# Performance work log

Measured on AMD Instinct MI355X. Metric: run time of the kernel, lower is better.

Reference implementation:

```python
import jax, jax.numpy as jnp
import numpy as np

HEADS, HEAD_SIZE, FREQS, MAX_PERIOD = 16, 64, 256, 10000
D_MODEL = 1024
NEG_INF = -1e9


def sinusoid_embedding(seq_len, frequencies, max_period):
    # Interleaved sin/cos sinusoid table, shape (seq_len, frequencies).
    pos = np.arange(seq_len, dtype=np.float64)[:, None]
    idx = np.arange(frequencies)[None, :]
    inv_freq = max_period ** (-(idx // 2 * 2) / frequencies)
    angle = pos * inv_freq
    table = np.where(idx % 2 == 0, np.sin(angle), np.cos(angle))
    return table.astype(np.float32)


def relative_causal(scores):
    # scores: (b, n, q, v) with v indexing relative distance d = q - k.
    # Returns a[..., q, k] = scores[..., q, q - k] (k > q entries are masked later).
    L = scores.shape[-1]
    d = jnp.clip(jnp.arange(L)[:, None] - jnp.arange(L)[None, :], 0, L - 1)  # (q, k)
    return jnp.take_along_axis(scores, d[None, None, :, :], axis=-1)


def setup_inputs() -> dict:
    key = jax.random.key(0)
    ks = jax.random.split(key, 4)
    u = np.sqrt(3.0)
    inp = jax.random.normal(ks[0], (2, 2048, D_MODEL), dtype=jnp.float32)
    qkv = jax.random.uniform(ks[1], (D_MODEL, 3, HEADS, HEAD_SIZE), jnp.float32, -u, u)
    q_bias = jnp.zeros((HEADS, HEAD_SIZE), jnp.float32)
    positional = jax.random.uniform(ks[2], (FREQS, HEADS, HEAD_SIZE), jnp.float32, -u, u)
    out_kernel = jax.random.uniform(ks[3], (HEADS * HEAD_SIZE, D_MODEL), jnp.float32, -u, u)
    out_bias = jnp.zeros((D_MODEL,), jnp.float32)
    return {"input": inp, "qkv": qkv, "q_bias": q_bias, "positional": positional,
            "out_kernel": out_kernel, "out_bias": out_bias}


def reference(input, qkv, q_bias, positional, out_kernel, out_bias):
    b, s, x = input.shape
    n, h = HEADS, HEAD_SIZE
    # QKV projection with unit-scaling forward factor.
    w = qkv * (3.0 * x * h * n) ** -0.25
    q, k, v = jnp.einsum('bsx,xAnh->Abnsh', input, w)  # each (b, n, s, h)
    q = q + q_bias[:, None, :]
    # Content scores.
    a = jnp.einsum('bnqh,bnkh->bnqk', q, k) * h ** -0.5
    # Relative-positional scores (Transformer-XL style).
    sins = jnp.asarray(np.sqrt(2.0) * sinusoid_embedding(s, FREQS, MAX_PERIOD))
    emb = jnp.einsum('sf,fnh->nsh', sins, positional * FREQS ** -0.5)
    pos_scores = jnp.einsum('bnqh,nvh->bnqv', q, emb) * h ** -0.5
    a = a + relative_causal(pos_scores)
    # Causal mask + softmax.
    mask = jnp.tril(jnp.ones((s, s), dtype=bool))
    a = jax.nn.softmax(jnp.where(mask, a, NEG_INF), axis=-1)
    # Weighted sum and output projection (Dense, scale_for='both').
    o = jnp.einsum('bnqk,bnkh->bqnh', a, v).reshape(b, s, n * h)
    fan_in, fan_out = out_kernel.shape
    out = o @ (out_kernel * (fan_in * fan_out) ** -0.25) + out_bias
    return out
```

## Files before the change

### kernel.cpp

```cpp
#include <hip/hip_runtime.h>
#include <math.h>

#define BATCH 2
#define SEQ 2048
#define DMODEL 1024
#define HEADS 16
#define HSIZE 64
#define FREQS 256
#define NH 1024
#define QKVN 3072

typedef __bf16 bf16;
typedef __bf16 bf16x8 __attribute__((ext_vector_type(8)));
typedef float f32x4 __attribute__((ext_vector_type(4)));

static __device__ __forceinline__ unsigned short bf16_bits(float v) {
    bf16 b = (bf16)v; return __builtin_bit_cast(unsigned short, b);
}

static __device__ __forceinline__ void gload16(const void* g, void* l) {
    __builtin_amdgcn_global_load_lds(
        (const __attribute__((address_space(1))) unsigned int*)g,
        (__attribute__((address_space(3))) unsigned int*)l, 16, 0, 0);
}

__global__ __launch_bounds__(256) void prep_kernel(
    const float* __restrict__ inp, const float* __restrict__ qkv_w,
    const float* __restrict__ out_kernel, const float* __restrict__ positional,
    bf16* __restrict__ a_bf, bf16* __restrict__ wt_qkv,
    bf16* __restrict__ wt_out, bf16* __restrict__ wt_pos,
    bf16* __restrict__ sins_bf)
{
    __shared__ float tile[32][33];
    const int id = blockIdx.x, t = threadIdx.x;

    if (id < 4096) {
        int i = id * 256 + t;
        float4 v = ((const float4*)inp)[i];
        ushort4 o;
        o.x = bf16_bits(v.x); o.y = bf16_bits(v.y);
        o.z = bf16_bits(v.z); o.w = bf16_bits(v.w);
        ((ushort4*)a_bf)[i] = o;
        return;
    }
    if (id < 6144) {
        int i = (id - 4096) * 256 + t;
        int s = i >> 8, f = i & 255;
        double e = -(double)((f >> 1) << 1) / (double)FREQS;
        double invf = pow(10000.0, e);
        double ang = (double)s * invf;
        double v = (f & 1) ? cos(ang) : sin(ang);
        sins_bf[i] = (bf16)(float)(1.4142135623730951 * v);
        return;
    }
    int id2 = id - 6144;
    const float* src; bf16* dst; int R, C, c0, r0;
    if (id2 < 3072) {
        src = qkv_w; dst = wt_qkv; R = 1024; C = 3072;
        c0 = (id2 % 96) * 32; r0 = (id2 / 96) * 32;
    } else if (id2 < 4096) {
        id2 -= 3072;
        src = out_kernel; dst = wt_out; R = 1024; C = 1024;
        c0 = (id2 & 31) * 32; r0 = (id2 >> 5) * 32;
    } else {
        id2 -= 4096;
        src = positional; dst = wt_pos; R = 256; C = 1024;
        c0 = (id2 & 31) * 32; r0 = (id2 >> 5) * 32;
    }
    const int tx = t & 31, ty = t >> 5;
#pragma unroll
    for (int i = 0; i < 4; i++)
        tile[ty + i * 8][tx] = src[(size_t)(r0 + ty + i * 8) * C + c0 + tx];
    __syncthreads();
#pragma unroll
    for (int i = 0; i < 4; i++)
        dst[(size_t)(c0 + ty + i * 8) * R + r0 + tx] = (bf16)tile[tx][ty + i * 8];
}

template<int EPI>
__global__ __launch_bounds__(256) void mfma_gemm(
    const bf16* __restrict__ A, const bf16* __restrict__ Bt,
    int K, float alpha, const float* __restrict__ bias,
    float* __restrict__ outf, bf16* __restrict__ ob0, bf16* __restrict__ ob1,
    bf16* __restrict__ ob2,
    const bf16* __restrict__ A2, const bf16* __restrict__ Bt2,
    bf16* __restrict__ ob3, float alpha2)
{
    __shared__ __align__(16) bf16 Atile[2][128 * 32];
    __shared__ __align__(16) bf16 Btile[2][128 * 32];

    const int t    = threadIdx.x;
    const int lane = t & 63;
    const int w    = t >> 6;
    const int quad = lane >> 4;
    const int l16  = lane & 15;
    const int wm   = (w >> 1) * 64;
    const int wn   = (w & 1) * 64;

    bool embp = false;
    int m0 = blockIdx.y * 128, n0 = blockIdx.x * 128, Kl = K;
    const bf16* Ap = A; const bf16* Btp = Bt; float al = alpha;
    if constexpr (EPI == 1) {
        if (blockIdx.x >= 24) {
            if (blockIdx.y >= 16) return;
            embp = true;
            n0 = (blockIdx.x - 24) * 128;
            Kl = FREQS; Ap = A2; Btp = Bt2; al = alpha2;
        }
    }
    const bool swapv = (EPI == 1) && !embp && (n0 >= 2048);

    const int rS = t >> 2;
    const int cS = (t & 3) ^ ((rS >> 1) & 3);
    const bf16* ag0 = Ap  + (size_t)(m0 + rS) * Kl + cS * 8;
    const bf16* ag1 = ag0 + (size_t)64 * Kl;
    const bf16* bg0 = Btp + (size_t)(n0 + rS) * Kl + cS * 8;
    const bf16* bg1 = bg0 + (size_t)64 * Kl;

    int aoff[4], boff[4];
#pragma unroll
    for (int mi = 0; mi < 4; ++mi) {
        int r = wm + mi * 16 + l16;
        aoff[mi] = r * 32 + ((quad ^ ((r >> 1) & 3)) * 8);
    }
#pragma unroll
    for (int ni = 0; ni < 4; ++ni) {
        int r = wn + ni * 16 + l16;
        boff[ni] = r * 32 + ((quad ^ ((r >> 1) & 3)) * 8);
    }

    gload16(ag0, (char*)Atile[0] + t * 16);
    gload16(ag1, (char*)Atile[0] + 4096 + t * 16);
    gload16(bg0, (char*)Btile[0] + t * 16);
    gload16(bg1, (char*)Btile[0] + 4096 + t * 16);

    const int nK = Kl >> 5;
    f32x4 acc[4][4] = {};

    for (int kk = 0; kk < nK; ++kk) {
        __syncthreads();
        if (kk + 1 < nK) {
            ag0 += 32; ag1 += 32; bg0 += 32; bg1 += 32;
            char* ad = (char*)Atile[(kk + 1) & 1];
            char* bd = (char*)Btile[(kk + 1) & 1];
            gload16(ag0, ad + t * 16); gload16(ag1, ad + 4096 + t * 16);
            gload16(bg0, bd + t * 16); gload16(bg1, bd + 4096 + t * 16);
        }
        const bf16* ab = Atile[kk & 1];
        const bf16* bb = Btile[kk & 1];
        bf16x8 af[4], bfr[4];
#pragma unroll
        for (int mi = 0; mi < 4; ++mi) af[mi] = *(const bf16x8*)(ab + aoff[mi]);
#pragma unroll
        for (int ni = 0; ni < 4; ++ni) bfr[ni] = *(const bf16x8*)(bb + boff[ni]);

        if (!swapv) {
#pragma unroll
            for (int mi = 0; mi < 4; ++mi)
#pragma unroll
                for (int ni = 0; ni < 4; ++ni)
                    acc[mi][ni] = __builtin_amdgcn_mfma_f32_16x16x32_bf16(
                        af[mi], bfr[ni], acc[mi][ni], 0, 0, 0);
        } else {
#pragma unroll
            for (int mi = 0; mi < 4; ++mi)
#pragma unroll
                for (int ni = 0; ni < 4; ++ni)
                    acc[mi][ni] = __builtin_amdgcn_mfma_f32_16x16x32_bf16(
                        bfr[ni], af[mi], acc[mi][ni], 0, 0, 0);
        }
    }

    if constexpr (EPI == 0) {
#pragma unroll
        for (int mi = 0; mi < 4; ++mi)
#pragma unroll
            for (int ni = 0; ni < 4; ++ni) {
                int col = n0 + wn + ni * 16 + l16;
                float bb = bias[col];
#pragma unroll
                for (int rg = 0; rg < 4; ++rg) {
                    int row = m0 + wm + mi * 16 + quad * 4 + rg;
                    outf[(size_t)row * NH + col] = acc[mi][ni][rg] * al + bb;
                }
            }
    } else {
        if (embp) {
#pragma unroll
            for (int mi = 0; mi < 4; ++mi)
#pragma unroll
                for (int ni = 0; ni < 4; ++ni) {
                    int col = n0 + wn + ni * 16 + l16;
                    int head = col >> 6, h = col & 63;
#pragma unroll
                    for (int rg = 0; rg < 4; ++rg) {
                        int d = m0 + wm + mi * 16 + quad * 4 + rg;
                        int hs = h ^ (((d + 63) & 7) << 3);
                        ob3[((size_t)(head * SEQ + d)) * 64 + hs] =
                            (bf16)(acc[mi][ni][rg] * al);
                    }
                }
        } else if (n0 >= 2048) {
#pragma unroll
            for (int mi = 0; mi < 4; ++mi)
#pragma unroll
                for (int ni = 0; ni < 4; ++ni) {
                    int mcol = m0 + wm + mi * 16 + l16;
                    int bb = mcol >> 11, s = mcol & 2047;
#pragma unroll
                    for (int rg = 0; rg < 4; ++rg) {
                        int hg = n0 + wn + ni * 16 + quad * 4 + rg;
                        int head = (hg & 1023) >> 6, h = hg & 63;
                        int ss = s ^ ((h & 7) << 3);
                        ob2[((size_t)((bb * 16 + head) * 64 + h)) * SEQ + ss] =
                            (bf16)(acc[mi][ni][rg] * al);
                    }
                }
        } else {
            const int whichk = (n0 >= 1024);
#pragma unroll
            for (int mi = 0; mi < 4; ++mi)
#pragma unroll
                for (int ni = 0; ni < 4; ++ni) {
                    int cg   = (n0 + wn + ni * 16 + l16) & 1023;
                    int head = cg >> 6, h = cg & 63;
                    float qbv = whichk ? 0.0f : bias[cg];
#pragma unroll
                    for (int rg = 0; rg < 4; ++rg) {
                        int row = m0 + wm + mi * 16 + quad * 4 + rg;
                        int bb = row >> 11, s = row & 2047;
                        float v = acc[mi][ni][rg] * al;
                        if (whichk) {
                            int hs = h ^ ((s & 7) << 3);
                            ob1[((size_t)((bb * 16 + head) * SEQ + s)) * 64 + hs] = (bf16)v;
                        } else {
                            ob0[((size_t)((bb * 16 + head) * SEQ + s)) * 64 + h] =
                                (bf16)((v + qbv) * 0.125f);
                        }
                    }
                }
        }
    }
}

__device__ const unsigned char YQC[24]  = {15,15,7,14,14,13,13,6,12,12,11,11,
                                           5,10,10,9,9,4,8,8,3,2,1,0};
__device__ const unsigned char YPRT[24] = {0,1,2,0,1,0,1,2,0,1,0,1,
                                           2,0,1,0,1,2,0,1,2,2,2,2};

__global__ __launch_bounds__(256, 2) void attn_kernel(
    const bf16* __restrict__ Qb, const bf16* __restrict__ Kb,
    const bf16* __restrict__ Vtb, const bf16* __restrict__ Eb,
    bf16* __restrict__ o, float* __restrict__ Opart, float* __restrict__ Lpart)
{
    __shared__ __align__(16) bf16 Ks[2][4096];
    __shared__ __align__(16) bf16 Vts[2][4096];
    __shared__ __align__(16) bf16 Es[256 * 64];
    __shared__ __align__(16) bf16 PS[4][16][72];

    const int t    = threadIdx.x;
    const int lane = t & 63;
    const int w    = t >> 6;
    const int quad = lane >> 4;
    const int l16  = lane & 15;

    const int bx = blockIdx.x;
    const int b  = bx >> 4, n = bx & 15;
    const int yy = blockIdx.y;
    const int qc = YQC[yy];
    const int pr = YPRT[yy];
    const int q0 = qc * 128;
    const int KT = 2 * qc + 2;
    const int kt0 = (pr == 1) ? (qc + 1) : 0;
    const int kt1 = (pr == 0) ? (qc + 1) : KT;
    const bool haspeel = (pr != 0);
    const bool split   = (pr != 2);
    const int qw0 = q0 + 16 * w;
    const int qw1 = qw0 + 64;

    const bf16* __restrict__ Qp = Qb  + (size_t)bx * SEQ * 64;
    const bf16* __restrict__ Kp = Kb  + (size_t)bx * SEQ * 64;
    const bf16* __restrict__ Vp = Vtb + (size_t)bx * SEQ * 64;
    const bf16* __restrict__ Ep = Eb  + (size_t)n  * SEQ * 64;

    const int key8 = (l16 & 7) << 3;
    const int ec0  = ((quad * 8) ^ key8) * 2;
    const int ec1  = ((32 + quad * 8) ^ key8) * 2;

    bf16x8 qf[2][2];
    qf[0][0] = *(const bf16x8*)(Qp + (size_t)(qw0 + l16) * 64 + quad * 8);
    qf[0][1] = *(const bf16x8*)(Qp + (size_t)(qw0 + l16) * 64 + 32 + quad * 8);
    qf[1][0] = *(const bf16x8*)(Qp + (size_t)(qw1 + l16) * 64 + quad * 8);
    qf[1][1] = *(const bf16x8*)(Qp + (size_t)(qw1 + l16) * 64 + 32 + quad * 8);

    int dsta[4];
    bool condp[4];
#pragma unroll
    for (int rg = 0; rg < 4; ++rg) {
        int rr   = quad * 4 + rg;
        int l16c = (rr + 15 - l16) & 15;
        dsta[rg]  = ((lane & 48) + l16c) << 2;
        condp[rg] = rr > l16c;
    }

    f32x4 O[2][4] = {};
    float lsum[2][4] = {};

    {
        const bf16* ksrc = Kp + kt0 * 4096;
        char* kd = (char*)Ks[kt0 & 1];
        char* vd = (char*)Vts[kt0 & 1];
        gload16(ksrc + t * 8,        kd + t * 16);
        gload16(ksrc + 2048 + t * 8, kd + 4096 + t * 16);
        gload16(Vp + (size_t)(t >> 3) * SEQ + kt0 * 64 + (t & 7) * 8,        vd + t * 16);
        gload16(Vp + (size_t)((t >> 3) + 32) * SEQ + kt0 * 64 + (t & 7) * 8, vd + 4096 + t * 16);
        const long D0 = (long)q0 - 64 * kt0 - 63;
        const int rI0 = (-64 * kt0) & 255;
#pragma unroll
        for (int g = 0; g < 6; ++g) {
            const int sI = (rI0 + 32 * g) & 255;
            gload16(Ep + (D0 + 32 * g) * 64 + t * 8, (char*)Es + sI * 128 + t * 16);
        }
    }

    auto load_kv = [&](const char* kb, const char* vb,
                       bf16x8 (&kf)[4][2], bf16x8 (&vf)[4][2]) {
#pragma unroll
        for (int j = 0; j < 4; ++j) {
            const char* kp = kb + (j * 16 + l16) * 128;
            kf[j][0] = *(const bf16x8*)(kp + ec0);
            kf[j][1] = *(const bf16x8*)(kp + ec1);
            const char* vp = vb + (j * 16 + l16) * 128;
            vf[j][0] = *(const bf16x8*)(vp + ec0);
            vf[j][1] = *(const bf16x8*)(vp + ec1);
        }
    };
    auto eread = [&](int rb, bf16x8 (&ef)[5][2]) {
#pragma unroll
        for (int jj = 0; jj < 5; ++jj) {
            const char* ep = (const char*)Es + ((rb + 16 * jj + l16) & 255) * 128;
            ef[jj][0] = *(const bf16x8*)(ep + ec0);
            ef[jj][1] = *(const bf16x8*)(ep + ec1);
        }
    };
    auto qkmfma = [&](const bf16x8 (&q2)[2], const bf16x8 (&kf)[4][2],
                      f32x4 (&S)[4]) {
#pragma unroll
        for (int j = 0; j < 4; ++j) {
            f32x4 a = {0, 0, 0, 0};
            a = __builtin_amdgcn_mfma_f32_16x16x32_bf16(q2[1], kf[j][1], a, 0, 0, 0);
            a = __builtin_amdgcn_mfma_f32_16x16x32_bf16(q2[0], kf[j][0], a, 0, 0, 0);
            S[j] = a;
        }
    };
    auto pamfma = [&](const bf16x8 (&q2)[2], const bf16x8 (&ef)[5][2],
                      f32x4 (&pa)[5]) {
#pragma unroll
        for (int jj = 0; jj < 5; ++jj) {
            f32x4 a = {0, 0, 0, 0};
            a = __builtin_amdgcn_mfma_f32_16x16x32_bf16(q2[1], ef[jj][1], a, 0, 0, 0);
            a = __builtin_amdgcn_mfma_f32_16x16x32_bf16(q2[0], ef[jj][0], a, 0, 0, 0);
            pa[jj] = a;
        }
    };
    auto smax = [&](int kq, f32x4 (&S)[4], const f32x4 (&pa)[5], float (&ls)[4]) {
#pragma unroll
        for (int j = 0; j < 4; ++j) {
#pragma unroll
            for (int rg = 0; rg < 4; ++rg) {
                float vsel = condp[rg] ? pa[4 - j][rg] : pa[3 - j][rg];
                int pv = __builtin_amdgcn_ds_permute(dsta[rg], __float_as_int(vsel));
                float sv = S[j][rg] + __int_as_float(pv);
                bool valid = (j * 16 + l16) <= (kq + quad * 4 + rg);
                S[j][rg] = valid ? __expf(sv) : 0.0f;
            }
        }
#pragma unroll
        for (int rg = 0; rg < 4; ++rg)
            ls[rg] += S[0][rg] + S[1][rg] + S[2][rg] + S[3][rg];
    };
    auto ps_write = [&](const f32x4 (&S)[4]) {
#pragma unroll
        for (int j = 0; j < 4; ++j)
#pragma unroll
            for (int rg = 0; rg < 4; ++rg)
                PS[w][quad * 4 + rg][j * 16 + l16] = (bf16)S[j][rg];
    };
    auto pvmfma = [&](const bf16x8 (&vf)[4][2], f32x4 (&Oc)[4]) {
        bf16x8 pf0 = *(const bf16x8*)(&PS[w][l16][quad * 8]);
        bf16x8 pf1 = *(const bf16x8*)(&PS[w][l16][32 + quad * 8]);
#pragma unroll
        for (int j4 = 0; j4 < 4; ++j4) {
            Oc[j4] = __builtin_amdgcn_mfma_f32_16x16x32_bf16(pf1, vf[j4][1], Oc[j4], 0, 0, 0);
            Oc[j4] = __builtin_amdgcn_mfma_f32_16x16x32_bf16(pf0, vf[j4][0], Oc[j4], 0, 0, 0);
        }
    };

    const int ktE = kt1 - (haspeel ? 1 : 0);
    for (int kt = kt0; kt < ktE; ++kt) {
        const int k0 = kt * 64;
        __syncthreads();

        const int nt = kt + 1;
        if (nt < kt1) {
            bf16* kd = Ks[nt & 1];
            bf16* vd = Vts[nt & 1];
            const bf16* ksrc = Kp + nt * 4096;
            gload16(ksrc + t * 8,        (char*)kd + t * 16);
            gload16(ksrc + 2048 + t * 8, (char*)kd + 4096 + t * 16);
            gload16(Vp + (size_t)(t >> 3) * SEQ + nt * 64 + (t & 7) * 8,
                    (char*)vd + t * 16);
            gload16(Vp + (size_t)((t >> 3) + 32) * SEQ + nt * 64 + (t & 7) * 8,
                    (char*)vd + 4096 + t * 16);
            const long d0 = (long)q0 - nt * 64 - 63;
            const int rI = (-64 * nt) & 255;
            gload16(Ep + d0 * 64 + t * 8,        (char*)Es + rI * 128 + t * 16);
            gload16(Ep + (d0 + 32) * 64 + t * 8, (char*)Es + rI * 128 + 4096 + t * 16);
        }

        bf16x8 kf[4][2], vf[4][2];
        load_kv((const char*)Ks[kt & 1], (const char*)Vts[kt & 1], kf, vf);

        bf16x8 ef0[5][2];
        eread(16 * w - k0, ef0);
        f32x4 S0[4], pa0[5];
        __builtin_amdgcn_s_setprio(1);
        qkmfma(qf[0], kf, S0);
        pamfma(qf[0], ef0, pa0);
        __builtin_amdgcn_s_setprio(0);
        smax(qw0 - k0, S0, pa0, lsum[0]);

        bf16x8 ef1[5][2];
        eread(16 * w + 64 - k0, ef1);
        ps_write(S0);

        f32x4 S1[4], pa1[5];
        __builtin_amdgcn_s_setprio(1);
        qkmfma(qf[1], kf, S1);
        pamfma(qf[1], ef1, pa1);
        pvmfma(vf, O[0]);
        __builtin_amdgcn_s_setprio(0);

        smax(qw1 - k0, S1, pa1, lsum[1]);
        ps_write(S1);
        __builtin_amdgcn_s_setprio(1);
        pvmfma(vf, O[1]);
        __builtin_amdgcn_s_setprio(0);
    }

    if (haspeel) {
        const int kt = kt1 - 1, k0 = kt * 64;
        __syncthreads();
        bf16x8 kf[4][2], vf[4][2];
        load_kv((const char*)Ks[kt & 1], (const char*)Vts[kt & 1], kf, vf);
        bf16x8 ef1[5][2];
        eread(16 * w + 64 - k0, ef1);
        f32x4 S1[4], pa1[5];
        qkmfma(qf[1], kf, S1);
        pamfma(qf[1], ef1, pa1);
        smax(qw1 - k0, S1, pa1, lsum[1]);
        ps_write(S1);
        pvmfma(vf, O[1]);
    }

    if (!split) {
#pragma unroll
        for (int c = 0; c < 2; ++c) {
#pragma unroll
            for (int rg = 0; rg < 4; ++rg) {
                float s = lsum[c][rg];
                s += __shfl_xor(s, 1);
                s += __shfl_xor(s, 2);
                s += __shfl_xor(s, 4);
                s += __shfl_xor(s, 8);
                float inv = 1.0f / s;
                int q = (c ? qw1 : qw0) + quad * 4 + rg;
                size_t ro = ((size_t)(b * SEQ + q)) * NH + n * 64;
                o[ro +  0 + l16] = (bf16)(O[c][0][rg] * inv);
                o[ro + 16 + l16] = (bf16)(O[c][1][rg] * inv);
                o[ro + 32 + l16] = (bf16)(O[c][2][rg] * inv);
                o[ro + 48 + l16] = (bf16)(O[c][3][rg] * inv);
            }
        }
    } else {
        const int pslot = pr;
        float* Ob = Opart + ((size_t)(pslot * 32 + bx)) * 1024 * 64;
        float* Lb = Lpart + ((size_t)(pslot * 32 + bx)) * 1024;
#pragma unroll
        for (int c = 0; c < 2; ++c) {
#pragma unroll
            for (int rg = 0; rg < 4; ++rg) {
                float s = lsum[c][rg];
                s += __shfl_xor(s, 1);
                s += __shfl_xor(s, 2);
                s += __shfl_xor(s, 4);
                s += __shfl_xor(s, 8);
                int q = (c ? qw1 : qw0) + quad * 4 + rg;
                int rloc = q - 1024;
                size_t ro = (size_t)rloc * 64;
                Ob[ro +  0 + l16] = O[c][0][rg];
                Ob[ro + 16 + l16] = O[c][1][rg];
                Ob[ro + 32 + l16] = O[c][2][rg];
                Ob[ro + 48 + l16] = O[c][3][rg];
                if (l16 == 0) Lb[rloc] = s;
            }
        }
    }
}

__global__ __launch_bounds__(256) void merge_kernel(
    const float* __restrict__ Opart, const float* __restrict__ Lpart,
    bf16* __restrict__ o)
{
    int idx = blockIdx.x * 256 + threadIdx.x;
    int h4 = idx & 15;
    int r  = (idx >> 4) & 1023;
    int bx = idx >> 14;
    size_t i0 = (((size_t)bx        * 1024 + r) * 64 + h4 * 4);
    size_t i1 = (((size_t)(32 + bx) * 1024 + r) * 64 + h4 * 4);
    float4 a = *(const float4*)(Opart + i0);
    float4 c = *(const float4*)(Opart + i1);
    float inv = 1.0f / (Lpart[bx * 1024 + r] + Lpart[32 * 1024 + bx * 1024 + r]);
    int b = bx >> 4, n = bx & 15;
    size_t ro = ((size_t)(b * SEQ + 1024 + r)) * NH + n * 64 + h4 * 4;
    ushort4 wv;
    wv.x = bf16_bits((a.x + c.x) * inv);
    wv.y = bf16_bits((a.y + c.y) * inv);
    wv.z = bf16_bits((a.z + c.z) * inv);
    wv.w = bf16_bits((a.w + c.w) * inv);
    *(ushort4*)(o + ro) = wv;
}

extern "C" void kernel_launch(void* const* d_in, const int* in_sizes, int n_in,
                              void* d_out, int out_size, void* d_ws, size_t ws_size,
                              hipStream_t stream) {
    const float* inp        = (const float*)d_in[0];
    const float* qkv_w      = (const float*)d_in[1];
    const float* q_bias     = (const float*)d_in[2];
    const float* positional = (const float*)d_in[3];
    const float* out_kernel = (const float*)d_in[4];
    const float* out_bias   = (const float*)d_in[5];

    char* p = (char*)d_ws;
    auto alloc = [&](size_t bytes) {
        char* q = p; p += (bytes + 255) & ~(size_t)255; return q;
    };
    bf16* qbuf    = (bf16*)alloc((size_t)BATCH * HEADS * SEQ * HSIZE * 2);
    bf16* kbuf    = (bf16*)alloc((size_t)BATCH * HEADS * SEQ * HSIZE * 2);
    bf16* vtbuf   = (bf16*)alloc((size_t)BATCH * HEADS * SEQ * HSIZE * 2);
    bf16* embT    = (bf16*)alloc((size_t)HEADS * SEQ * HSIZE * 2);
    bf16* sins_bf = (bf16*)alloc((size_t)SEQ * FREQS * 2);
    bf16* obuf    = (bf16*)alloc((size_t)BATCH * SEQ * NH * 2);
    bf16* wt_out  = (bf16*)alloc((size_t)NH * DMODEL * 2);
    bf16* wt_pos  = (bf16*)alloc((size_t)NH * FREQS * 2);
    bf16* a_bf    = (bf16*)alloc((size_t)BATCH * SEQ * DMODEL * 2);
    bf16* wt_qkv  = (bf16*)alloc((size_t)QKVN * DMODEL * 2);
    (void)       alloc((size_t)2097152);
    float* Opart  = (float*)a_bf;
    float* Lpart  = (float*)wt_pos;

    const float qkv_scale = (float)pow(3.0 * DMODEL * HSIZE * HEADS, -0.25);
    const float emb_scale = 0.0625f;
    const float out_scale = 0.03125f;

    prep_kernel<<<10496, 256, 0, stream>>>(
        inp, qkv_w, out_kernel, positional, a_bf, wt_qkv, wt_out, wt_pos, sins_bf);

    mfma_gemm<1><<<dim3(32, 32), 256, 0, stream>>>(
        a_bf, wt_qkv, DMODEL, qkv_scale, q_bias, nullptr, qbuf, kbuf, vtbuf,
        sins_bf, wt_pos, embT, emb_scale);

    attn_kernel<<<dim3(32, 24), 256, 0, stream>>>(
        qbuf, kbuf, vtbuf, embT, obuf, Opart, Lpart);

    merge_kernel<<<2048, 256, 0, stream>>>(Opart, Lpart, obuf);

    mfma_gemm<0><<<dim3(8, 32), 256, 0, stream>>>(
        obuf, wt_out, DMODEL, out_scale, out_bias, (float*)d_out,
        nullptr, nullptr, nullptr, nullptr, nullptr, nullptr, 0.0f);
}
```

Before: 259.1 us.

## Triple-buffer GEMM LDS tiles with explicit vmcnt waits for deeper prefetch

The MFMA GEMM moves from double to triple buffering of its A/B LDS tiles. Global-to-LDS loads are now issued two k-steps ahead, and each step waits with an explicit s_waitcnt vmcnt(4) plus a raw s_barrier instead of __syncthreads. The aim is to hide more global-load latency behind the MFMA work. In exchange, LDS use per block grows by half (to 48KB), which may cut occupancy. The hand-placed waitcnt and barrier also depend on how the compiler orders memory operations.

```diff
diff --git a/kernel.cpp b/kernel.cpp
--- a/kernel.cpp
+++ b/kernel.cpp
@@ -86,8 +86,8 @@
     const bf16* __restrict__ A2, const bf16* __restrict__ Bt2,
     bf16* __restrict__ ob3, float alpha2)
 {
-    __shared__ __align__(16) bf16 Atile[2][128 * 32];
-    __shared__ __align__(16) bf16 Btile[2][128 * 32];
+    __shared__ __align__(16) bf16 Atile[3][128 * 32];
+    __shared__ __align__(16) bf16 Btile[3][128 * 32];
 
     const int t    = threadIdx.x;
     const int lane = t & 63;
@@ -117,6 +117,16 @@
     const bf16* bg0 = Btp + (size_t)(n0 + rS) * Kl + cS * 8;
     const bf16* bg1 = bg0 + (size_t)64 * Kl;
 
+    auto stage = [&](int ks) {
+        char* ad = (char*)Atile[ks % 3];
+        char* bd = (char*)Btile[ks % 3];
+        const int ko = ks * 32;
+        gload16(ag0 + ko, ad + t * 16);
+        gload16(ag1 + ko, ad + 4096 + t * 16);
+        gload16(bg0 + ko, bd + t * 16);
+        gload16(bg1 + ko, bd + 4096 + t * 16);
+    };
+
     int aoff[4], boff[4];
 #pragma unroll
     for (int mi = 0; mi < 4; ++mi) {
@@ -129,30 +139,27 @@
         boff[ni] = r * 32 + ((quad ^ ((r >> 1) & 3)) * 8);
     }
 
-    gload16(ag0, (char*)Atile[0] + t * 16);
-    gload16(ag1, (char*)Atile[0] + 4096 + t * 16);
-    gload16(bg0, (char*)Btile[0] + t * 16);
-    gload16(bg1, (char*)Btile[0] + 4096 + t * 16);
-
     const int nK = Kl >> 5;
+    stage(0);
+    stage(1);
+
     f32x4 acc[4][4] = {};
 
     for (int kk = 0; kk < nK; ++kk) {
-        __syncthreads();
-        if (kk + 1 < nK) {
-            ag0 += 32; ag1 += 32; bg0 += 32; bg1 += 32;
-            char* ad = (char*)Atile[(kk + 1) & 1];
-            char* bd = (char*)Btile[(kk + 1) & 1];
-            gload16(ag0, ad + t * 16); gload16(ag1, ad + 4096 + t * 16);
-            gload16(bg0, bd + t * 16); gload16(bg1, bd + 4096 + t * 16);
-        }
-        const bf16* ab = Atile[kk & 1];
-        const bf16* bb = Btile[kk & 1];
+        if (kk + 1 < nK) asm volatile("s_waitcnt vmcnt(4)" ::: "memory");
+        else             asm volatile("s_waitcnt vmcnt(0)" ::: "memory");
+        __builtin_amdgcn_s_barrier();
+        __builtin_amdgcn_sched_barrier(0);
+
+        const bf16* ab = Atile[kk % 3];
+        const bf16* bb = Btile[kk % 3];
         bf16x8 af[4], bfr[4];
 #pragma unroll
         for (int mi = 0; mi < 4; ++mi) af[mi] = *(const bf16x8*)(ab + aoff[mi]);
 #pragma unroll
         for (int ni = 0; ni < 4; ++ni) bfr[ni] = *(const bf16x8*)(bb + boff[ni]);
+
+        if (kk + 2 < nK) stage(kk + 2);
 
         if (!swapv) {
 #pragma unroll
```

Result: faster. 243.6 us (-6.0%).
